# Kernel optimization log

Hardware: AMD Instinct MI355X
Metric: run time of the kernel (lower is better)

The kernel has to match this reference:

```python
import jax, jax.numpy as jnp
import numpy as np

RADII = (4, 8, 16)
BETA = 0.3
TEMP = 0.07
EPS = 1e-6


def box_filter(x, r):
    """Windowed sum over a (2r+1)x(2r+1) window with zero padding (same as
    F.conv2d with a ones kernel and padding=r), applied to the last two axes.
    Uses cumulative sums (integral image) instead of an explicit convolution."""
    def along(x, axis):
        n = x.shape[axis]
        c = jnp.cumsum(x, axis=axis)
        pad = [(0, 0)] * x.ndim
        pad[axis] = (1, 0)
        c = jnp.pad(c, pad)  # prepend a zero so c[i] = sum of first i elems
        i = jnp.arange(n)
        hi = jnp.clip(i + r + 1, 0, n)
        lo = jnp.clip(i - r, 0, n)
        return jnp.take(c, hi, axis=axis) - jnp.take(c, lo, axis=axis)
    return along(along(x, -2), -1)


def build_prototypes(support_feats, mask_f, anchor_pos, anchor_sample, anchor_radius):
    """mask_f: [S,H,W] float. Returns (local_protos [M,C], local_weights [M], global_proto [C])."""
    fg = mask_f.sum()
    global_proto = (support_feats * mask_f[:, None]).sum((0, 2, 3)) / (fg + EPS)

    masked = support_feats * mask_f[:, None]  # [S,C,H,W]
    means, msums = [], []
    for r in RADII:
        fsum = box_filter(masked, r)              # [S,C,H,W] windowed masked feature sum
        msum = box_filter(mask_f, r)              # [S,H,W]   windowed fg pixel count
        means.append(fsum / (msum[:, None] + EPS))
        msums.append(msum)
    mean = jnp.stack(means)   # [R,S,C,H,W] windowed masked means per radius
    msum = jnp.stack(msums)   # [R,S,H,W]

    y, x = anchor_pos[:, 0], anchor_pos[:, 1]
    local_protos = mean[anchor_radius, anchor_sample, :, y, x]   # [M,C]
    local_weights = msum[anchor_radius, anchor_sample, y, x]     # [M]
    local_weights = local_weights / (local_weights.sum() + EPS)
    return local_protos, local_weights, global_proto


def _l2norm(x, axis):
    n = jnp.sqrt(jnp.sum(x * x, axis=axis, keepdims=True))
    return x / jnp.maximum(n, 1e-12)


def reference(support_feats, support_masks, query_feats, anchor_pos, anchor_sample, anchor_radius):
    mask_f = support_masks.astype(support_feats.dtype)[:, 0]  # [S,H,W]
    protos, weights, gproto = build_prototypes(
        support_feats, mask_f, anchor_pos, anchor_sample, anchor_radius)

    q_norm = _l2norm(query_feats, axis=1)                     # [B,C,H,W]
    g = _l2norm(gproto[None], axis=1)[0]                      # [C]
    s_global = jnp.einsum('bchw,c->bhw', q_norm, g)

    p_norm = _l2norm(protos, axis=1)                          # [M,C]
    sims = jnp.einsum('bchw,mc->bmhw', q_norm, p_norm)        # [B,M,H,W]
    w = weights / (weights.sum() + EPS)
    local_score = jnp.einsum('bmhw,m->bhw', sims, w)

    s_fg = BETA * s_global + (1.0 - BETA) * local_score
    logits = jnp.stack((-s_fg / TEMP, s_fg / TEMP), axis=1)   # [B,2,H,W]
    return logits


def setup_inputs() -> dict:
    key = jax.random.key(0)
    k1, k2, k3, k4, k5, k6 = jax.random.split(key, 6)
    S, C, H, W = 4, 384, 96, 96
    B, M = 8, 64
    return {
        'support_feats': jax.random.normal(k1, (S, C, H, W), dtype=jnp.float32),
        'support_masks': jax.random.randint(k2, (S, 1, H, W), 0, 2, dtype=jnp.int32),
        'query_feats': jax.random.normal(k3, (B, C, H, W), dtype=jnp.float32),
        'anchor_pos': jax.random.randint(k4, (M, 2), 0, H, dtype=jnp.int32),
        'anchor_sample': jax.random.randint(k5, (M,), 0, S, dtype=jnp.int32),
        'anchor_radius': jax.random.randint(k6, (M,), 0, len(RADII), dtype=jnp.int32),
    }
```

## Files before the change

### kernel.cpp

```cpp
#include <hip/hip_runtime.h>
#include <hip/hip_bf16.h>
#include <math.h>

#define S_ 4
#define C_ 384
#define H_ 96
#define W_ 96
#define B_ 8
#define M_ 64
#define HW_ (H_ * W_)
#define EPSV 1e-6f
#define BETA_V 0.3f
#define TEMP_V 0.07f

#define NB_A (S_ * C_)
#define NB_B (M_ * (C_ / 4))
#define NB_PREP (NB_A + NB_B + 1)

__device__ __forceinline__ float wave_sum(float v) {
#pragma unroll
    for (int o = 32; o; o >>= 1) v += __shfl_down(v, o, 64);
    return v;
}

__device__ __forceinline__ float block_sum(float v) {
    __shared__ float sm[8];
    int lane = threadIdx.x & 63;
    int wid = threadIdx.x >> 6;
    v = wave_sum(v);
    if (lane == 0) sm[wid] = v;
    __syncthreads();
    float r = 0.0f;
#pragma unroll
    for (int i = 0; i < 4; ++i) r += sm[i];
    __syncthreads();
    return r;
}

__global__ __launch_bounds__(256) void k_prep(const float* __restrict__ feats,
                                              const int* __restrict__ mask,
                                              const int* __restrict__ pos,
                                              const int* __restrict__ samp,
                                              const int* __restrict__ rad,
                                              float* __restrict__ partial,
                                              float* __restrict__ proto,
                                              float* __restrict__ msum_out,
                                              float* __restrict__ fg_out) {
    int bid = blockIdx.x;
    int t = threadIdx.x;

    if (bid < NB_A) {
        int s = bid / C_;
        const float4* fp = (const float4*)(feats + (size_t)bid * HW_);
        const int4* mp = (const int4*)(mask + (size_t)s * HW_);
        float acc = 0.0f;
        for (int i = t; i < HW_ / 4; i += 256) {
            float4 f = fp[i];
            int4 m = mp[i];
            acc += f.x * (float)m.x + f.y * (float)m.y + f.z * (float)m.z + f.w * (float)m.w;
        }
        float tot = block_sum(acc);
        if (t == 0) partial[bid] = tot;
        return;
    }
    bid -= NB_A;
    if (bid < NB_B) {
        const int CG = C_ / 4;
        int m = bid / CG;
        int cg = bid % CG;
        int y = pos[2 * m + 0];
        int x = pos[2 * m + 1];
        int s = samp[m];
        int ri = rad[m];
        int r = (ri == 0) ? 4 : (ri == 1) ? 8 : 16;
        int y0 = max(y - r, 0), y1 = min(y + r + 1, H_);
        int x0 = max(x - r, 0), x1 = min(x + r + 1, W_);
        int ww = x1 - x0;
        int n = (y1 - y0) * ww;

        __shared__ float mwin[33 * 33];
        const int* mp = mask + (size_t)s * HW_;
        float macc = 0.0f;
        {
            int yy = t / ww;
            int xx = t - yy * ww;
            int dy = 256 / ww, dx = 256 - dy * ww;
            for (int i = t; i < n; i += 256) {
                float mv = (float)mp[(y0 + yy) * W_ + x0 + xx];
                mwin[i] = mv;
                macc += mv;
                xx += dx; yy += dy;
                if (xx >= ww) { xx -= ww; ++yy; }
            }
        }
        float msumv = block_sum(macc);
        if (cg == 0 && t == 0) msum_out[m] = msumv;
        float inv = 1.0f / (msumv + EPSV);

        int wid = t >> 6;
        int lane = t & 63;
        int c = cg * 4 + wid;
        const float* fp = feats + ((size_t)s * C_ + c) * HW_;
        float acc = 0.0f;
        {
            int yy = lane / ww;
            int xx = lane - yy * ww;
            int dy = 64 / ww, dx = 64 - dy * ww;
            for (int i = lane; i < n; i += 64) {
                acc += fp[(y0 + yy) * W_ + x0 + xx] * mwin[i];
                xx += dx; yy += dy;
                if (xx >= ww) { xx -= ww; ++yy; }
            }
        }
        acc = wave_sum(acc);
        if (lane == 0) proto[m * C_ + c] = acc * inv;
        return;
    }
    const int4* mp4 = (const int4*)mask;
    float acc = 0.0f;
    for (int i = t; i < S_ * HW_ / 4; i += 256) {
        int4 m = mp4[i];
        acc += (float)(m.x + m.y + m.z + m.w);
    }
    float fg = block_sum(acc);
    if (t == 0) fg_out[0] = fg;
}

__global__ __launch_bounds__(256) void k_finalize(const float* __restrict__ partial,
                                                  const float* __restrict__ msum,
                                                  const float* __restrict__ proto,
                                                  const float* __restrict__ fg_in,
                                                  float* __restrict__ v) {
    int tid = threadIdx.x;
    int wid = tid >> 6;
    int lane = tid & 63;

    float invfg = 1.0f / (fg_in[0] + EPSV);

    __shared__ float gv[C_];
    for (int c = tid; c < C_; c += 256) {
        float tv = 0.0f;
        for (int s = 0; s < S_; ++s) tv += partial[s * C_ + c];
        gv[c] = tv * invfg;
    }
    __syncthreads();

    float sq = 0.0f;
    for (int c = tid; c < C_; c += 256) sq += gv[c] * gv[c];
    float gn = block_sum(sq);
    gn = fmaxf(sqrtf(gn), 1e-12f);

    float wa = (tid < M_) ? msum[tid] : 0.0f;
    float T = block_sum(wa);
    float wb = (tid < M_) ? msum[tid] / (T + EPSV) : 0.0f;
    float wsum = block_sum(wb);

    __shared__ float pn[M_];
    for (int m = wid; m < M_; m += 4) {
        float a = 0.0f;
        for (int c = lane; c < C_; c += 64) {
            float p = proto[m * C_ + c];
            a += p * p;
        }
        a = wave_sum(a);
        if (lane == 0) pn[m] = fmaxf(sqrtf(a), 1e-12f);
    }
    __syncthreads();

    __shared__ float wq[M_];
    if (tid < M_) {
        float w = (msum[tid] / (T + EPSV)) / (wsum + EPSV);
        wq[tid] = w / pn[tid];
    }
    __syncthreads();

    for (int c = tid; c < C_; c += 256) {
        float vl = 0.0f;
        for (int m = 0; m < M_; ++m) vl += wq[m] * proto[m * C_ + c];
        v[c] = BETA_V * (gv[c] / gn) + (1.0f - BETA_V) * vl;
    }
}

__global__ __launch_bounds__(256) void k_score(const float* __restrict__ q,
                                               const float* __restrict__ v,
                                               float* __restrict__ out) {
    __shared__ float vs[C_];
    for (int c = threadIdx.x; c < C_; c += 256) vs[c] = v[c];
    __syncthreads();

    int wid = threadIdx.x >> 6;
    int lane = threadIdx.x & 63;
    int pixbase = blockIdx.x * 256;
    int b = pixbase / HW_;
    int p0 = pixbase - b * HW_;
    const float4* qp = (const float4*)(q + ((size_t)b * C_ + wid * 96) * HW_ + p0);

    float4 dot = {0.f, 0.f, 0.f, 0.f};
    float4 sq = {0.f, 0.f, 0.f, 0.f};
#pragma unroll 8
    for (int c = 0; c < 96; ++c) {
        float4 f = qp[(size_t)c * (HW_ / 4) + lane];
        float vc = vs[wid * 96 + c];
        dot.x += f.x * vc; dot.y += f.y * vc; dot.z += f.z * vc; dot.w += f.w * vc;
        sq.x += f.x * f.x; sq.y += f.y * f.y; sq.z += f.z * f.z; sq.w += f.w * f.w;
    }

    __shared__ float4 sd[4][64];
    __shared__ float4 ss[4][64];
    sd[wid][lane] = dot;
    ss[wid][lane] = sq;
    __syncthreads();
    if (wid == 0) {
        float4 d = sd[0][lane];
        float4 s2 = ss[0][lane];
#pragma unroll
        for (int w = 1; w < 4; ++w) {
            float4 a = sd[w][lane];
            float4 b2 = ss[w][lane];
            d.x += a.x; d.y += a.y; d.z += a.z; d.w += a.w;
            s2.x += b2.x; s2.y += b2.y; s2.z += b2.z; s2.w += b2.w;
        }
        float4 o;
        o.x = (d.x / fmaxf(sqrtf(s2.x), 1e-12f)) / TEMP_V;
        o.y = (d.y / fmaxf(sqrtf(s2.y), 1e-12f)) / TEMP_V;
        o.z = (d.z / fmaxf(sqrtf(s2.z), 1e-12f)) / TEMP_V;
        o.w = (d.w / fmaxf(sqrtf(s2.w), 1e-12f)) / TEMP_V;
        float4 no = {-o.x, -o.y, -o.z, -o.w};
        float* ob = out + (size_t)b * 2 * HW_;
        ((float4*)(ob + p0))[lane] = no;
        ((float4*)(ob + HW_ + p0))[lane] = o;
    }
}

extern "C" void kernel_launch(void* const* d_in, const int* in_sizes, int n_in,
                              void* d_out, int out_size, void* d_ws, size_t ws_size,
                              hipStream_t stream) {
    const float* support_feats = (const float*)d_in[0];
    const int* support_masks = (const int*)d_in[1];
    const float* query_feats = (const float*)d_in[2];
    const int* anchor_pos = (const int*)d_in[3];
    const int* anchor_sample = (const int*)d_in[4];
    const int* anchor_radius = (const int*)d_in[5];
    float* out = (float*)d_out;

    float* ws = (float*)d_ws;
    float* ws_partial = ws;
    float* ws_msum = ws_partial + S_ * C_;
    float* ws_proto = ws_msum + M_;
    float* ws_v = ws_proto + M_ * C_;
    float* ws_fg = ws_v + C_;

    k_prep<<<NB_PREP, 256, 0, stream>>>(support_feats, support_masks, anchor_pos,
                                        anchor_sample, anchor_radius,
                                        ws_partial, ws_proto, ws_msum, ws_fg);
    k_finalize<<<1, 256, 0, stream>>>(ws_partial, ws_msum, ws_proto, ws_fg, ws_v);
    k_score<<<B_ * HW_ / 256, 256, 0, stream>>>(query_feats, ws_v, out);
}
```

Measured before the change: 95.97 us.

## Split query scoring across channel slices and coarsen prototype channel work

```diff
diff --git a/kernel.cpp b/kernel.cpp
--- a/kernel.cpp
+++ b/kernel.cpp
@@ -1,5 +1,4 @@
 #include <hip/hip_runtime.h>
-#include <hip/hip_bf16.h>
 #include <math.h>
 
 #define S_ 4
@@ -14,8 +13,15 @@
 #define TEMP_V 0.07f
 
 #define NB_A (S_ * C_)
-#define NB_B (M_ * (C_ / 4))
+#define CGB 64
+#define NB_B (M_ * (C_ / CGB))
 #define NB_PREP (NB_A + NB_B + 1)
+
+#define NSLICE 4
+#define CS (C_ / NSLICE)
+#define NTILE (HW_ / 256)
+#define NB_S1 (B_ * NSLICE * NTILE)
+#define NB_S2 (B_ * HW_ / 256)
 
 __device__ __forceinline__ float wave_sum(float v) {
 #pragma unroll
@@ -24,15 +30,13 @@
 }
 
 __device__ __forceinline__ float block_sum(float v) {
-    __shared__ float sm[8];
+    __shared__ float sm[4];
     int lane = threadIdx.x & 63;
     int wid = threadIdx.x >> 6;
     v = wave_sum(v);
     if (lane == 0) sm[wid] = v;
     __syncthreads();
-    float r = 0.0f;
-#pragma unroll
-    for (int i = 0; i < 4; ++i) r += sm[i];
+    float r = sm[0] + sm[1] + sm[2] + sm[3];
     __syncthreads();
     return r;
 }
@@ -54,7 +58,9 @@
         const float4* fp = (const float4*)(feats + (size_t)bid * HW_);
         const int4* mp = (const int4*)(mask + (size_t)s * HW_);
         float acc = 0.0f;
-        for (int i = t; i < HW_ / 4; i += 256) {
+#pragma unroll
+        for (int k = 0; k < HW_ / 4 / 256; ++k) {
+            int i = t + k * 256;
             float4 f = fp[i];
             int4 m = mp[i];
             acc += f.x * (float)m.x + f.y * (float)m.y + f.z * (float)m.z + f.w * (float)m.w;
@@ -65,9 +71,9 @@
     }
     bid -= NB_A;
     if (bid < NB_B) {
-        const int CG = C_ / 4;
-        int m = bid / CG;
-        int cg = bid % CG;
+        const int NCG = C_ / CGB;
+        int m = bid / NCG;
+        int cg = bid % NCG;
         int y = pos[2 * m + 0];
         int x = pos[2 * m + 1];
         int s = samp[m];
@@ -99,21 +105,39 @@
 
         int wid = t >> 6;
         int lane = t & 63;
-        int c = cg * 4 + wid;
-        const float* fp = feats + ((size_t)s * C_ + c) * HW_;
-        float acc = 0.0f;
-        {
+        int cbase = cg * CGB + wid * 16;
+        const float* fbase = feats + (size_t)s * C_ * HW_;
+        for (int jb = 0; jb < 4; ++jb) {
+            int c0 = cbase + jb * 4;
+            const float* f0 = fbase + (size_t)(c0 + 0) * HW_;
+            const float* f1 = fbase + (size_t)(c0 + 1) * HW_;
+            const float* f2 = fbase + (size_t)(c0 + 2) * HW_;
+            const float* f3 = fbase + (size_t)(c0 + 3) * HW_;
+            float a0 = 0.f, a1 = 0.f, a2 = 0.f, a3 = 0.f;
             int yy = lane / ww;
             int xx = lane - yy * ww;
             int dy = 64 / ww, dx = 64 - dy * ww;
             for (int i = lane; i < n; i += 64) {
-                acc += fp[(y0 + yy) * W_ + x0 + xx] * mwin[i];
+                int off = (y0 + yy) * W_ + x0 + xx;
+                float mv = mwin[i];
+                a0 += f0[off] * mv;
+                a1 += f1[off] * mv;
+                a2 += f2[off] * mv;
+                a3 += f3[off] * mv;
                 xx += dx; yy += dy;
                 if (xx >= ww) { xx -= ww; ++yy; }
             }
-        }
-        acc = wave_sum(acc);
-        if (lane == 0) proto[m * C_ + c] = acc * inv;
+            a0 = wave_sum(a0);
+            a1 = wave_sum(a1);
+            a2 = wave_sum(a2);
+            a3 = wave_sum(a3);
+            if (lane == 0) {
+                proto[m * C_ + c0 + 0] = a0 * inv;
+                proto[m * C_ + c0 + 1] = a1 * inv;
+                proto[m * C_ + c0 + 2] = a2 * inv;
+                proto[m * C_ + c0 + 3] = a3 * inv;
+            }
+        }
         return;
     }
     const int4* mp4 = (const int4*)mask;
@@ -181,26 +205,30 @@
     }
 }
 
-__global__ __launch_bounds__(256) void k_score(const float* __restrict__ q,
-                                               const float* __restrict__ v,
-                                               float* __restrict__ out) {
-    __shared__ float vs[C_];
-    for (int c = threadIdx.x; c < C_; c += 256) vs[c] = v[c];
-    __syncthreads();
+__global__ __launch_bounds__(256) void k_score1(const float* __restrict__ q,
+                                                const float* __restrict__ v,
+                                                float* __restrict__ wsd,
+                                                float* __restrict__ wss) {
+    int bid = blockIdx.x;
+    int tile = bid % NTILE;
+    int bs = bid / NTILE;
+    int sl = bs % NSLICE;
+    int b = bs / NSLICE;
 
     int wid = threadIdx.x >> 6;
     int lane = threadIdx.x & 63;
-    int pixbase = blockIdx.x * 256;
-    int b = pixbase / HW_;
-    int p0 = pixbase - b * HW_;
-    const float4* qp = (const float4*)(q + ((size_t)b * C_ + wid * 96) * HW_ + p0);
+    int p0 = tile * 256;
+
+    const float4* qp = (const float4*)(q + (size_t)b * C_ * HW_ + p0);
+    int c0 = sl * CS + wid * 24;
 
     float4 dot = {0.f, 0.f, 0.f, 0.f};
     float4 sq = {0.f, 0.f, 0.f, 0.f};
 #pragma unroll 8
-    for (int c = 0; c < 96; ++c) {
+    for (int j = 0; j < 24; ++j) {
+        int c = c0 + j;
         float4 f = qp[(size_t)c * (HW_ / 4) + lane];
-        float vc = vs[wid * 96 + c];
+        float vc = v[c];
         dot.x += f.x * vc; dot.y += f.y * vc; dot.z += f.z * vc; dot.w += f.w * vc;
         sq.x += f.x * f.x; sq.y += f.y * f.y; sq.z += f.z * f.z; sq.w += f.w * f.w;
     }
@@ -220,16 +248,31 @@
             d.x += a.x; d.y += a.y; d.z += a.z; d.w += a.w;
             s2.x += b2.x; s2.y += b2.y; s2.z += b2.z; s2.w += b2.w;
         }
-        float4 o;
-        o.x = (d.x / fmaxf(sqrtf(s2.x), 1e-12f)) / TEMP_V;
-        o.y = (d.y / fmaxf(sqrtf(s2.y), 1e-12f)) / TEMP_V;
-        o.z = (d.z / fmaxf(sqrtf(s2.z), 1e-12f)) / TEMP_V;
-        o.w = (d.w / fmaxf(sqrtf(s2.w), 1e-12f)) / TEMP_V;
-        float4 no = {-o.x, -o.y, -o.z, -o.w};
-        float* ob = out + (size_t)b * 2 * HW_;
-        ((float4*)(ob + p0))[lane] = no;
-        ((float4*)(ob + HW_ + p0))[lane] = o;
-    }
+        size_t base = ((size_t)(b * NSLICE + sl) * HW_ + p0) / 4;
+        ((float4*)wsd)[base + lane] = d;
+        ((float4*)wss)[base + lane] = s2;
+    }
+}
+
+__global__ __launch_bounds__(256) void k_score2(const float* __restrict__ wsd,
+                                                const float* __restrict__ wss,
+                                                float* __restrict__ out) {
+    int px = blockIdx.x * 256 + threadIdx.x;
+    int b = px / HW_;
+    int p = px - b * HW_;
+
+    float d = 0.0f, s2 = 0.0f;
+#pragma unroll
+    for (int sl = 0; sl < NSLICE; ++sl) {
+        size_t idx = (size_t)(b * NSLICE + sl) * HW_ + p;
+        d += wsd[idx];
+        s2 += wss[idx];
+    }
+    float sv = d / fmaxf(sqrtf(s2), 1e-12f);
+    float o = sv / TEMP_V;
+    float* ob = out + (size_t)b * 2 * HW_;
+    ob[p] = -o;
+    ob[HW_ + p] = o;
 }
 
 extern "C" void kernel_launch(void* const* d_in, const int* in_sizes, int n_in,
@@ -249,10 +292,13 @@
     float* ws_proto = ws_msum + M_;
     float* ws_v = ws_proto + M_ * C_;
     float* ws_fg = ws_v + C_;
+    float* ws_dot = ws_fg + 1;
+    float* ws_sq = ws_dot + B_ * NSLICE * HW_;
 
     k_prep<<<NB_PREP, 256, 0, stream>>>(support_feats, support_masks, anchor_pos,
                                         anchor_sample, anchor_radius,
                                         ws_partial, ws_proto, ws_msum, ws_fg);
     k_finalize<<<1, 256, 0, stream>>>(ws_partial, ws_msum, ws_proto, ws_fg, ws_v);
-    k_score<<<B_ * HW_ / 256, 256, 0, stream>>>(query_feats, ws_v, out);
-}
+    k_score1<<<NB_S1, 256, 0, stream>>>(query_feats, ws_v, ws_dot, ws_sq);
+    k_score2<<<NB_S2, 256, 0, stream>>>(ws_dot, ws_sq, out);
+}
```

Result: slower. 103.7 us (+8.1%).
